# Performance work log

Hardware: AMD Instinct MI355X
Metric: run time of the kernel (lower is better)

## Reference

```python
import jax, jax.numpy as jnp
import numpy as np

N_NODES = 50000
N_EDGES = 200000
NODE_F = 64
EDGE_F = 16
HID = 32
LAT = 16


def _glorot(key, shape):
    fan_in, fan_out = shape[0], shape[1]
    lim = np.sqrt(6.0 / (fan_in + fan_out))
    return jax.random.uniform(key, shape, jnp.float32, -lim, lim)


def setup_inputs() -> dict:
    key = jax.random.key(0)
    ks = jax.random.split(key, 24)
    inp = {
        "x": jax.random.normal(ks[0], (N_NODES, NODE_F), jnp.float32),
        "edge_index": jax.random.randint(ks[1], (2, N_EDGES), 0, N_NODES, jnp.int64),
        "edge_attr": jax.random.normal(ks[2], (N_EDGES, EDGE_F), jnp.float32),
        # encoder input projection
        "lin_in_w": _glorot(ks[3], (NODE_F, HID)),
        "lin_in_b": jnp.zeros((HID,), jnp.float32),
        # 3 edge MLPs (stacked over layer axis)
        "edge_w1": jnp.stack([_glorot(ks[4 + i], (EDGE_F, HID)) for i in range(3)]),
        "edge_b1": jnp.zeros((3, HID), jnp.float32),
        "edge_w2": jnp.stack([_glorot(ks[7 + i], (HID, HID * HID)) * 0.1 for i in range(3)]),
        "edge_b2": jnp.zeros((3, HID * HID), jnp.float32),
        # 3 NNConv root weights + biases
        "root_w": jnp.stack([_glorot(ks[10 + i], (HID, HID)) for i in range(3)]),
        "root_b": jnp.zeros((3, HID), jnp.float32),
        # encoder output projection
        "lin_out_w": _glorot(ks[13], (HID, LAT)),
        "lin_out_b": jnp.zeros((LAT,), jnp.float32),
        # node decoder MLP
        "dec_w1": _glorot(ks[14], (LAT, HID)),
        "dec_b1": jnp.zeros((HID,), jnp.float32),
        "dec_w2": _glorot(ks[15], (HID, NODE_F)),
        "dec_b2": jnp.zeros((NODE_F,), jnp.float32),
    }
    return inp


def _nnconv(x, src, dst, edge_attr, w1, b1, w2, b2, root_w, root_b):
    # per-edge weight matrix from edge MLP: [E, H, H]
    h = jax.nn.relu(edge_attr @ w1 + b1)
    w_e = (h @ w2 + b2).reshape(-1, HID, HID)
    # gather source features, per-edge matmul: [E, H]
    msg = jnp.einsum("eh,eho->eo", x[src], w_e)
    # scatter-mean to destinations
    agg = jax.ops.segment_sum(msg, dst, num_segments=N_NODES)
    cnt = jax.ops.segment_sum(jnp.ones((msg.shape[0], 1), x.dtype), dst, num_segments=N_NODES)
    agg = agg / jnp.maximum(cnt, 1.0)
    # root weight + bias
    return agg + x @ root_w + root_b


def reference(x, edge_index, edge_attr, lin_in_w, lin_in_b, edge_w1, edge_b1,
              edge_w2, edge_b2, root_w, root_b, lin_out_w, lin_out_b,
              dec_w1, dec_b1, dec_w2, dec_b2):
    src, dst = edge_index[0], edge_index[1]
    h = jax.nn.relu(x @ lin_in_w + lin_in_b)
    for i in range(3):  # fixed number of conv layers (dropout is identity in eval)
        h = _nnconv(h, src, dst, edge_attr, edge_w1[i], edge_b1[i],
                    edge_w2[i], edge_b2[i], root_w[i], root_b[i])
        h = jax.nn.relu(h)
    z = h @ lin_out_w + lin_out_b
    # node decoder
    d = jax.nn.relu(z @ dec_w1 + dec_b1)
    return d @ dec_w2 + dec_b2
```

## Files before the change

kernel.cpp:

```cpp
#include <hip/hip_runtime.h>
#include <hip/hip_bf16.h>
#include <stdint.h>

#define N_NODES 50000
#define N_EDGES 200000
#define NODE_F 64
#define EDGE_F 16
#define HID 32
#define LAT 16
#define KTOT 1056
#define SCAN_BLOCKS 196

typedef __attribute__((ext_vector_type(8))) short short8;
typedef __attribute__((ext_vector_type(4))) float f32x4;
typedef __attribute__((ext_vector_type(2))) float f32x2;

static __device__ __forceinline__ unsigned short bfbits(float f) {
  union { __hip_bfloat16 h; unsigned short s; } c; c.h = __float2bfloat16(f); return c.s;
}
static __device__ __forceinline__ unsigned pkt(f32x2 v) {
  return __builtin_amdgcn_perm(__float_as_uint(v.y), __float_as_uint(v.x), 0x07060302u);
}
union AFrag { short8 v; unsigned u[4]; };

__global__ void k_prep(const float* __restrict__ ew2, const float* __restrict__ eb2,
                       const float* __restrict__ ew1,
                       unsigned short* __restrict__ w2t,
                       unsigned short* __restrict__ w1p,
                       int* __restrict__ deg) {
  int g = blockIdx.x*256 + threadIdx.x;
  int l = g / (HID*KTOT);
  int r = g % (HID*KTOT);
  int o = r / KTOT;
  int kg = r % KTOT;
  int k = kg >> 5, h = kg & 31;
  float v = (k < 32) ? ew2[(size_t)l*32768 + k*1024 + h*32 + o]
                     : eb2[(size_t)l*1024 + h*32 + o];
  w2t[g] = bfbits(v);
  if (g < N_NODES) deg[g] = 0;
  if (g < 3*2*64*8) {
    int l2 = g >> 10;
    int r2 = g & 1023;
    int nt = r2 >> 9;
    int ln = (r2 >> 3) & 63;
    int j  = r2 & 7;
    int kgr = ln >> 4;
    float w = (kgr < 2) ? ew1[(size_t)l2*512 + (kgr*8 + j)*32 + nt*16 + (ln & 15)] : 0.f;
    w1p[g] = bfbits(w);
  }
}

__global__ void k_hist(const int* __restrict__ ei, int* __restrict__ deg) {
  int t = blockIdx.x*256 + threadIdx.x;
  if (t >= N_EDGES) return;
  int d = ei[N_EDGES + t];
  d = min(max(d, 0), N_NODES-1);
  atomicAdd(&deg[d], 1);
}

__global__ __launch_bounds__(256) void k_scan1(const int* __restrict__ deg,
                                               int* __restrict__ off,
                                               int* __restrict__ bsum) {
  __shared__ int s[256];
  const int tid = threadIdx.x;
  const int t = blockIdx.x*256 + tid;
  int d = (t < N_NODES) ? deg[t] : 0;
  s[tid] = d; __syncthreads();
  int v = d;
  #pragma unroll
  for (int ofs = 1; ofs < 256; ofs <<= 1) {
    int w = (tid >= ofs) ? s[tid-ofs] : 0;
    __syncthreads();
    v += w; s[tid] = v;
    __syncthreads();
  }
  if (t < N_NODES) off[t] = v - d;
  if (tid == 255) bsum[blockIdx.x] = v;
}

__global__ __launch_bounds__(256) void k_scan23(int* __restrict__ off,
                                                const int* __restrict__ bsum,
                                                int* __restrict__ cursor) {
  __shared__ int sPref;
  const int tid = threadIdx.x;
  const int b = blockIdx.x;
  if (tid < 64) {
    int acc = 0;
    for (int i = tid; i < b; i += 64) acc += bsum[i];
    #pragma unroll
    for (int o = 32; o; o >>= 1) acc += __shfl_down(acc, o);
    if (tid == 0) sPref = acc;
  }
  __syncthreads();
  int pref = sPref;
  int t = b*256 + tid;
  if (t < N_NODES) {
    off[t] += pref;
    cursor[t] = 0;
  }
  if (t == 0) off[N_NODES] = N_EDGES;
}

__global__ void k_scatter(const int* __restrict__ ei, const int* __restrict__ off,
                          int* __restrict__ cursor, int* __restrict__ csr_pos) {
  int t = blockIdx.x*256 + threadIdx.x;
  if (t >= N_EDGES) return;
  int d = ei[N_EDGES + t];
  d = min(max(d, 0), N_NODES-1);
  int pos = atomicAdd(&cursor[d], 1);
  csr_pos[t] = off[d] + pos;
}

__global__ void k_lin_in(const float* __restrict__ x,
                         const float* __restrict__ W,
                         const float* __restrict__ b,
                         float* __restrict__ h) {
  __shared__ float Ws[NODE_F*HID];
  __shared__ float bs[HID];
  for (int i = threadIdx.x; i < NODE_F*HID; i += 256) Ws[i] = W[i];
  if (threadIdx.x < HID) bs[threadIdx.x] = b[threadIdx.x];
  __syncthreads();
  int t = blockIdx.x*256 + threadIdx.x;
  if (t >= N_NODES*HID) return;
  int n = t >> 5, o = t & 31;
  const float4* xp = (const float4*)(x + (size_t)n*NODE_F);
  float acc = bs[o];
  #pragma unroll
  for (int j = 0; j < NODE_F/4; j++) {
    float4 v = xp[j];
    acc = fmaf(v.x, Ws[(4*j+0)*HID+o], acc);
    acc = fmaf(v.y, Ws[(4*j+1)*HID+o], acc);
    acc = fmaf(v.z, Ws[(4*j+2)*HID+o], acc);
    acc = fmaf(v.w, Ws[(4*j+3)*HID+o], acc);
  }
  h[t] = fmaxf(acc, 0.f);
}

__global__ __launch_bounds__(256) void k_msg(const float* __restrict__ hin,
                                             const float* __restrict__ ea,
                                             const int* __restrict__ ei,
                                             const unsigned short* __restrict__ w1pl,
                                             const float* __restrict__ b1,
                                             const unsigned short* __restrict__ w2tl,
                                             const int* __restrict__ csr_pos,
                                             unsigned short* __restrict__ msgB) {
  __shared__ float sHE[256*33];
  __shared__ int   sSRC[256];
  __shared__ int   sPOS[256];
  const int tid = threadIdx.x;
  const int be  = blockIdx.x*256;
  const int wv   = tid >> 6;
  const int lane = tid & 63;
  const int nn   = lane & 15;
  const int quad = lane >> 4;
  const int wbase = wv*64;

  {
    int el = wbase + lane;
    int e = min(be + el, N_EDGES-1);
    sSRC[el] = min(max(ei[e], 0), N_NODES-1);
    sPOS[el] = csr_pos[e];
    sHE[el*33 + 32] = 1.0f;
  }

  {
    short8 wb0 = *(const short8*)(w1pl + lane*8);
    short8 wb1 = *(const short8*)(w1pl + 512 + lane*8);
    f32x4 z = {0.f,0.f,0.f,0.f};
    float bv0 = b1[nn], bv1 = b1[nn + 16];
    #pragma unroll
    for (int t = 0; t < 4; t++) {
      AFrag a;
      if (quad < 2) {
        int e = min(be + wbase + t*16 + nn, N_EDGES-1);
        const float4* p = (const float4*)(ea + (size_t)e*EDGE_F + quad*8);
        float4 u = p[0], v = p[1];
        a.u[0] = pkt(f32x2{u.x,u.y}); a.u[1] = pkt(f32x2{u.z,u.w});
        a.u[2] = pkt(f32x2{v.x,v.y}); a.u[3] = pkt(f32x2{v.z,v.w});
      } else {
        #pragma unroll
        for (int i = 0; i < 4; i++) a.u[i] = 0u;
      }
      f32x4 h0 = __builtin_amdgcn_mfma_f32_16x16x32_bf16(a.v, wb0, z, 0, 0, 0);
      f32x4 h1 = __builtin_amdgcn_mfma_f32_16x16x32_bf16(a.v, wb1, z, 0, 0, 0);
      #pragma unroll
      for (int r = 0; r < 4; r++) {
        int ro = (wbase + t*16 + quad*4 + r)*33;
        sHE[ro + nn]      = fmaxf(h0[r] + bv0, 0.f);
        sHE[ro + 16 + nn] = fmaxf(h1[r] + bv1, 0.f);
      }
    }
  }

  f32x2 xs[4][4];
  #pragma unroll
  for (int t = 0; t < 4; t++) {
    int si = sSRC[wbase + t*16 + nn];
    const float4* p = (const float4*)(hin + (size_t)si*HID);
    float4 a = p[quad*2], b = p[quad*2+1];
    xs[t][0] = f32x2{a.x, a.y}; xs[t][1] = f32x2{a.z, a.w};
    xs[t][2] = f32x2{b.x, b.y}; xs[t][3] = f32x2{b.z, b.w};
  }

  f32x4 c0[4], c1[4];
  #pragma unroll
  for (int t = 0; t < 4; t++) { c0[t] = f32x4{0.f,0.f,0.f,0.f}; c1[t] = c0[t]; }

  const unsigned short* bp0 = w2tl + (unsigned)nn*KTOT + quad*8;
  const unsigned short* bp1 = bp0 + 16*KTOT;
  const float* heR[4];
  #pragma unroll
  for (int t = 0; t < 4; t++) heR[t] = sHE + (wbase + t*16 + nn)*33;

  short8 sb0[3], sb1[3];
  float  sh[3][4];
  #pragma unroll
  for (int j = 0; j < 3; j++) {
    sb0[j] = *(const short8*)(bp0 + j*32);
    sb1[j] = *(const short8*)(bp1 + j*32);
    #pragma unroll
    for (int t = 0; t < 4; t++) sh[j][t] = heR[t][j];
  }

  #pragma unroll 1
  for (int base = 0; base < 30; base += 3) {
    #pragma unroll
    for (int j = 0; j < 3; j++) {
      const int kk = base + j;
      short8 cb0 = sb0[j], cb1 = sb1[j];
      #pragma unroll
      for (int t = 0; t < 4; t++) {
        float hk = sh[j][t];
        AFrag a;
        #pragma unroll
        for (int i = 0; i < 4; i++) a.u[i] = pkt(xs[t][i]*hk);
        c0[t] = __builtin_amdgcn_mfma_f32_16x16x32_bf16(a.v, cb0, c0[t], 0, 0, 0);
        c1[t] = __builtin_amdgcn_mfma_f32_16x16x32_bf16(a.v, cb1, c1[t], 0, 0, 0);
      }
      sb0[j] = *(const short8*)(bp0 + (kk+3)*32);
      sb1[j] = *(const short8*)(bp1 + (kk+3)*32);
      #pragma unroll
      for (int t = 0; t < 4; t++) sh[j][t] = heR[t][kk+3];
    }
  }
  #pragma unroll
  for (int j = 0; j < 3; j++) {
    short8 cb0 = sb0[j], cb1 = sb1[j];
    #pragma unroll
    for (int t = 0; t < 4; t++) {
      float hk = sh[j][t];
      AFrag a;
      #pragma unroll
      for (int i = 0; i < 4; i++) a.u[i] = pkt(xs[t][i]*hk);
      c0[t] = __builtin_amdgcn_mfma_f32_16x16x32_bf16(a.v, cb0, c0[t], 0, 0, 0);
      c1[t] = __builtin_amdgcn_mfma_f32_16x16x32_bf16(a.v, cb1, c1[t], 0, 0, 0);
    }
  }

  #pragma unroll
  for (int t = 0; t < 4; t++) {
    #pragma unroll
    for (int r = 0; r < 4; r++) {
      int el = wbase + t*16 + quad*4 + r;
      if (be + el < N_EDGES) {
        size_t row = (size_t)sPOS[el]*HID;
        msgB[row +      nn] = bfbits(c0[t][r]);
        msgB[row + 16 + nn] = bfbits(c1[t][r]);
      }
    }
  }
}

__global__ void k_gather(const unsigned short* __restrict__ msgB,
                         const int* __restrict__ off,
                         const float* __restrict__ hin,
                         const float* __restrict__ rw,
                         const float* __restrict__ rb,
                         float* __restrict__ hout) {
  __shared__ float rws[HID*HID];
  __shared__ float rbs[HID];
  for (int i = threadIdx.x; i < HID*HID; i += 256) rws[i] = rw[i];
  if (threadIdx.x < HID) rbs[threadIdx.x] = rb[threadIdx.x];
  __syncthreads();
  int t = blockIdx.x*256 + threadIdx.x;
  if (t >= N_NODES*8) return;
  int n = t >> 3, oc = t & 7;
  int s0 = off[n], s1 = off[n+1];
  float a0 = 0.f, a1 = 0.f, a2 = 0.f, a3 = 0.f;
  for (int j = s0; j < s1; j++) {
    uint2 u = *(const uint2*)(msgB + (size_t)j*HID + oc*4);
    a0 += __uint_as_float(u.x << 16);
    a1 += __uint_as_float(u.x & 0xffff0000u);
    a2 += __uint_as_float(u.y << 16);
    a3 += __uint_as_float(u.y & 0xffff0000u);
  }
  float inv = 1.f / fmaxf((float)(s1 - s0), 1.f);
  a0 = fmaf(a0, inv, rbs[oc*4+0]);
  a1 = fmaf(a1, inv, rbs[oc*4+1]);
  a2 = fmaf(a2, inv, rbs[oc*4+2]);
  a3 = fmaf(a3, inv, rbs[oc*4+3]);
  const float4* hp = (const float4*)(hin + (size_t)n*HID);
  #pragma unroll
  for (int jq = 0; jq < 8; jq++) {
    float4 hv = hp[jq];
    #pragma unroll
    for (int c = 0; c < 4; c++) {
      int j = jq*4 + c;
      float h = (c==0)?hv.x:(c==1)?hv.y:(c==2)?hv.z:hv.w;
      const float4* rp = (const float4*)(rws + j*HID + oc*4);
      float4 r = rp[0];
      a0 = fmaf(h, r.x, a0);
      a1 = fmaf(h, r.y, a1);
      a2 = fmaf(h, r.z, a2);
      a3 = fmaf(h, r.w, a3);
    }
  }
  float4 res = make_float4(fmaxf(a0,0.f), fmaxf(a1,0.f), fmaxf(a2,0.f), fmaxf(a3,0.f));
  ((float4*)(hout + (size_t)n*HID))[oc] = res;
}

__global__ void k_decoder(const float* __restrict__ h,
                          const float* __restrict__ lo_w, const float* __restrict__ lo_b,
                          const float* __restrict__ d1_w, const float* __restrict__ d1_b,
                          const float* __restrict__ d2_w, const float* __restrict__ d2_b,
                          float* __restrict__ out) {
  __shared__ float lows[HID*LAT], lobs[LAT], d1s[LAT*HID], d1bs[HID], d2s[HID*NODE_F], d2bs[NODE_F];
  for (int i = threadIdx.x; i < HID*LAT; i += 256) lows[i] = lo_w[i];
  for (int i = threadIdx.x; i < LAT; i += 256) lobs[i] = lo_b[i];
  for (int i = threadIdx.x; i < LAT*HID; i += 256) d1s[i] = d1_w[i];
  for (int i = threadIdx.x; i < HID; i += 256) d1bs[i] = d1_b[i];
  for (int i = threadIdx.x; i < HID*NODE_F; i += 256) d2s[i] = d2_w[i];
  for (int i = threadIdx.x; i < NODE_F; i += 256) d2bs[i] = d2_b[i];
  __syncthreads();
  int n = blockIdx.x*256 + threadIdx.x;
  if (n >= N_NODES) return;
  float hr[HID];
  const float4* hp = (const float4*)(h + (size_t)n*HID);
  #pragma unroll
  for (int i = 0; i < HID/4; i++) { float4 v = hp[i]; hr[4*i]=v.x; hr[4*i+1]=v.y; hr[4*i+2]=v.z; hr[4*i+3]=v.w; }
  float z[LAT];
  #pragma unroll
  for (int o = 0; o < LAT; o++) {
    float a = lobs[o];
    #pragma unroll
    for (int j = 0; j < HID; j++) a = fmaf(hr[j], lows[j*LAT+o], a);
    z[o] = a;
  }
  float d[HID];
  #pragma unroll
  for (int o = 0; o < HID; o++) {
    float a = d1bs[o];
    #pragma unroll
    for (int j = 0; j < LAT; j++) a = fmaf(z[j], d1s[j*HID+o], a);
    d[o] = fmaxf(a, 0.f);
  }
  float* op = out + (size_t)n*NODE_F;
  #pragma unroll 8
  for (int o = 0; o < NODE_F; o++) {
    float a = d2bs[o];
    #pragma unroll
    for (int j = 0; j < HID; j++) a = fmaf(d[j], d2s[j*NODE_F+o], a);
    op[o] = a;
  }
}

extern "C" void kernel_launch(void* const* d_in, const int* in_sizes, int n_in,
                              void* d_out, int out_size, void* d_ws, size_t ws_size,
                              hipStream_t stream) {
  const float* x   = (const float*)d_in[0];
  const int*   ei  = (const int*)d_in[1];
  const float* ea  = (const float*)d_in[2];
  const float* liw = (const float*)d_in[3];
  const float* lib = (const float*)d_in[4];
  const float* ew1 = (const float*)d_in[5];
  const float* eb1 = (const float*)d_in[6];
  const float* ew2 = (const float*)d_in[7];
  const float* eb2 = (const float*)d_in[8];
  const float* rw  = (const float*)d_in[9];
  const float* rb  = (const float*)d_in[10];
  const float* low = (const float*)d_in[11];
  const float* lob = (const float*)d_in[12];
  const float* d1w = (const float*)d_in[13];
  const float* d1b = (const float*)d_in[14];
  const float* d2w = (const float*)d_in[15];
  const float* d2b = (const float*)d_in[16];
  float* out = (float*)d_out;

  float* h0   = (float*)d_ws;
  float* h1   = h0  + (size_t)N_NODES*HID;
  unsigned short* msgB = (unsigned short*)(h1 + (size_t)N_NODES*HID);
  int*  deg   = (int*)(msgB + (size_t)N_EDGES*HID);
  int*  off   = deg + N_NODES;
  int*  cursor= off + N_NODES + 16;
  int*  cpos  = cursor + N_NODES;
  int*  bsum  = cpos + N_EDGES;
  unsigned short* w2t = (unsigned short*)(bsum + 256);
  unsigned short* w1p = w2t + 3*HID*KTOT;

  k_prep<<<(3*HID*KTOT)/256, 256, 0, stream>>>(ew2, eb2, ew1, w2t, w1p, deg);
  k_hist<<<(N_EDGES + 255)/256, 256, 0, stream>>>(ei, deg);
  k_scan1<<<SCAN_BLOCKS, 256, 0, stream>>>(deg, off, bsum);
  k_scan23<<<SCAN_BLOCKS, 256, 0, stream>>>(off, bsum, cursor);
  k_scatter<<<(N_EDGES + 255)/256, 256, 0, stream>>>(ei, off, cursor, cpos);

  k_lin_in<<<(N_NODES*HID + 255)/256, 256, 0, stream>>>(x, liw, lib, h0);

  float* hin = h0; float* hout = h1;
  for (int i = 0; i < 3; i++) {
    k_msg<<<(N_EDGES + 255)/256, 256, 0, stream>>>(hin, ea, ei,
        w1p + (size_t)i*1024, eb1 + i*HID,
        w2t + (size_t)i*HID*KTOT, cpos, msgB);
    k_gather<<<(N_NODES*8 + 255)/256, 256, 0, stream>>>(msgB, off, hin,
        rw + i*HID*HID, rb + i*HID, hout);
    float* t = hin; hin = hout; hout = t;
  }

  k_decoder<<<(N_NODES + 255)/256, 256, 0, stream>>>(hin, low, lob, d1w, d1b, d2w, d2b, out);
}
```

Before: 276.3 us.

## Reorder per-edge message contraction: MFMA over weights times x, then scale by h

The per-edge message is recomputed as a sum over k of h_k times (W2_k^T x), with W2 as the A operand and the gathered source features as a fixed B fragment. This replaces the per-k scaling and bf16 packing of x by h_k with FMAs on the MFMA outputs, using MFMA with a zero accumulator. The weight layout is rebuilt in prep to match the A-fragment format, and message stores become packed 8-byte writes. In exchange it adds VALU FMAs per MFMA output element, and the extra dependency on each MFMA result could stall the pipeline.

Measured after the change: 282.7 us. 2.3% more time.

```diff
diff --git a/kernel.cpp b/kernel.cpp
--- a/kernel.cpp
+++ b/kernel.cpp
@@ -9,6 +9,7 @@
 #define HID 32
 #define LAT 16
 #define KTOT 1056
+#define W2A_L 33792
 #define SCAN_BLOCKS 196
 
 typedef __attribute__((ext_vector_type(8))) short short8;
@@ -25,27 +26,31 @@
 
 __global__ void k_prep(const float* __restrict__ ew2, const float* __restrict__ eb2,
                        const float* __restrict__ ew1,
-                       unsigned short* __restrict__ w2t,
+                       unsigned short* __restrict__ w2a,
                        unsigned short* __restrict__ w1p,
                        int* __restrict__ deg) {
   int g = blockIdx.x*256 + threadIdx.x;
-  int l = g / (HID*KTOT);
-  int r = g % (HID*KTOT);
-  int o = r / KTOT;
-  int kg = r % KTOT;
-  int k = kg >> 5, h = kg & 31;
-  float v = (k < 32) ? ew2[(size_t)l*32768 + k*1024 + h*32 + o]
-                     : eb2[(size_t)l*1024 + h*32 + o];
-  w2t[g] = bfbits(v);
+  int l = g / W2A_L;
+  int r = g % W2A_L;
+  int k = r >> 10;
+  int r2 = r & 1023;
+  int mt = r2 >> 9;
+  int ln = (r2 >> 3) & 63;
+  int j  = r2 & 7;
+  int h  = (ln >> 4)*8 + j;
+  int m  = mt*16 + (ln & 15);
+  float v = (k < 32) ? ew2[(size_t)l*32768 + k*1024 + h*32 + m]
+                     : eb2[(size_t)l*1024 + h*32 + m];
+  w2a[g] = bfbits(v);
   if (g < N_NODES) deg[g] = 0;
   if (g < 3*2*64*8) {
     int l2 = g >> 10;
-    int r2 = g & 1023;
-    int nt = r2 >> 9;
-    int ln = (r2 >> 3) & 63;
-    int j  = r2 & 7;
-    int kgr = ln >> 4;
-    float w = (kgr < 2) ? ew1[(size_t)l2*512 + (kgr*8 + j)*32 + nt*16 + (ln & 15)] : 0.f;
+    int r3 = g & 1023;
+    int nt = r3 >> 9;
+    int ln2 = (r3 >> 3) & 63;
+    int j2  = r3 & 7;
+    int kgr = ln2 >> 4;
+    float w = (kgr < 2) ? ew1[(size_t)l2*512 + (kgr*8 + j2)*32 + nt*16 + (ln2 & 15)] : 0.f;
     w1p[g] = bfbits(w);
   }
 }
@@ -141,7 +146,7 @@
                                              const int* __restrict__ ei,
                                              const unsigned short* __restrict__ w1pl,
                                              const float* __restrict__ b1,
-                                             const unsigned short* __restrict__ w2tl,
+                                             const unsigned short* __restrict__ w2al,
                                              const int* __restrict__ csr_pos,
                                              unsigned short* __restrict__ msgB) {
   __shared__ float sHE[256*33];
@@ -192,32 +197,34 @@
     }
   }
 
-  f32x2 xs[4][4];
+  short8 bx[4];
   #pragma unroll
   for (int t = 0; t < 4; t++) {
     int si = sSRC[wbase + t*16 + nn];
-    const float4* p = (const float4*)(hin + (size_t)si*HID);
-    float4 a = p[quad*2], b = p[quad*2+1];
-    xs[t][0] = f32x2{a.x, a.y}; xs[t][1] = f32x2{a.z, a.w};
-    xs[t][2] = f32x2{b.x, b.y}; xs[t][3] = f32x2{b.z, b.w};
+    const float4* p = (const float4*)(hin + (size_t)si*HID + quad*8);
+    float4 a = p[0], b = p[1];
+    AFrag f;
+    f.u[0] = pkt(f32x2{a.x,a.y}); f.u[1] = pkt(f32x2{a.z,a.w});
+    f.u[2] = pkt(f32x2{b.x,b.y}); f.u[3] = pkt(f32x2{b.z,b.w});
+    bx[t] = f.v;
   }
 
   f32x4 c0[4], c1[4];
   #pragma unroll
   for (int t = 0; t < 4; t++) { c0[t] = f32x4{0.f,0.f,0.f,0.f}; c1[t] = c0[t]; }
-
-  const unsigned short* bp0 = w2tl + (unsigned)nn*KTOT + quad*8;
-  const unsigned short* bp1 = bp0 + 16*KTOT;
+  const f32x4 zz = {0.f,0.f,0.f,0.f};
+
+  const unsigned short* ap = w2al + (unsigned)lane*8;
   const float* heR[4];
   #pragma unroll
   for (int t = 0; t < 4; t++) heR[t] = sHE + (wbase + t*16 + nn)*33;
 
-  short8 sb0[3], sb1[3];
+  short8 sa0[3], sa1[3];
   float  sh[3][4];
   #pragma unroll
   for (int j = 0; j < 3; j++) {
-    sb0[j] = *(const short8*)(bp0 + j*32);
-    sb1[j] = *(const short8*)(bp1 + j*32);
+    sa0[j] = *(const short8*)(ap + j*1024);
+    sa1[j] = *(const short8*)(ap + j*1024 + 512);
     #pragma unroll
     for (int t = 0; t < 4; t++) sh[j][t] = heR[t][j];
   }
@@ -227,46 +234,51 @@
     #pragma unroll
     for (int j = 0; j < 3; j++) {
       const int kk = base + j;
-      short8 cb0 = sb0[j], cb1 = sb1[j];
+      short8 a0 = sa0[j], a1 = sa1[j];
       #pragma unroll
       for (int t = 0; t < 4; t++) {
+        f32x4 u0 = __builtin_amdgcn_mfma_f32_16x16x32_bf16(a0, bx[t], zz, 0, 0, 0);
+        f32x4 u1 = __builtin_amdgcn_mfma_f32_16x16x32_bf16(a1, bx[t], zz, 0, 0, 0);
         float hk = sh[j][t];
-        AFrag a;
         #pragma unroll
-        for (int i = 0; i < 4; i++) a.u[i] = pkt(xs[t][i]*hk);
-        c0[t] = __builtin_amdgcn_mfma_f32_16x16x32_bf16(a.v, cb0, c0[t], 0, 0, 0);
-        c1[t] = __builtin_amdgcn_mfma_f32_16x16x32_bf16(a.v, cb1, c1[t], 0, 0, 0);
+        for (int r = 0; r < 4; r++) {
+          c0[t][r] = fmaf(hk, u0[r], c0[t][r]);
+          c1[t][r] = fmaf(hk, u1[r], c1[t][r]);
+        }
       }
-      sb0[j] = *(const short8*)(bp0 + (kk+3)*32);
-      sb1[j] = *(const short8*)(bp1 + (kk+3)*32);
+      sa0[j] = *(const short8*)(ap + (kk+3)*1024);
+      sa1[j] = *(const short8*)(ap + (kk+3)*1024 + 512);
       #pragma unroll
       for (int t = 0; t < 4; t++) sh[j][t] = heR[t][kk+3];
     }
   }
   #pragma unroll
   for (int j = 0; j < 3; j++) {
-    short8 cb0 = sb0[j], cb1 = sb1[j];
+    short8 a0 = sa0[j], a1 = sa1[j];
     #pragma unroll
     for (int t = 0; t < 4; t++) {
+      f32x4 u0 = __builtin_amdgcn_mfma_f32_16x16x32_bf16(a0, bx[t], zz, 0, 0, 0);
+      f32x4 u1 = __builtin_amdgcn_mfma_f32_16x16x32_bf16(a1, bx[t], zz, 0, 0, 0);
       float hk = sh[j][t];
-      AFrag a;
       #pragma unroll
-      for (int i = 0; i < 4; i++) a.u[i] = pkt(xs[t][i]*hk);
-      c0[t] = __builtin_amdgcn_mfma_f32_16x16x32_bf16(a.v, cb0, c0[t], 0, 0, 0);
-      c1[t] = __builtin_amdgcn_mfma_f32_16x16x32_bf16(a.v, cb1, c1[t], 0, 0, 0);
+      for (int r = 0; r < 4; r++) {
+        c0[t][r] = fmaf(hk, u0[r], c0[t][r]);
+        c1[t][r] = fmaf(hk, u1[r], c1[t][r]);
+      }
     }
   }
 
   #pragma unroll
   for (int t = 0; t < 4; t++) {
-    #pragma unroll
-    for (int r = 0; r < 4; r++) {
-      int el = wbase + t*16 + quad*4 + r;
-      if (be + el < N_EDGES) {
-        size_t row = (size_t)sPOS[el]*HID;
-        msgB[row +      nn] = bfbits(c0[t][r]);
-        msgB[row + 16 + nn] = bfbits(c1[t][r]);
-      }
+    int el = wbase + t*16 + nn;
+    if (be + el < N_EDGES) {
+      size_t row = (size_t)sPOS[el]*HID;
+      unsigned a0 = bfbits(c0[t][0]) | ((unsigned)bfbits(c0[t][1]) << 16);
+      unsigned a1 = bfbits(c0[t][2]) | ((unsigned)bfbits(c0[t][3]) << 16);
+      unsigned b0 = bfbits(c1[t][0]) | ((unsigned)bfbits(c1[t][1]) << 16);
+      unsigned b1v = bfbits(c1[t][2]) | ((unsigned)bfbits(c1[t][3]) << 16);
+      *(uint2*)(msgB + row + quad*4)      = make_uint2(a0, a1);
+      *(uint2*)(msgB + row + 16 + quad*4) = make_uint2(b0, b1v);
     }
   }
 }
@@ -394,10 +406,10 @@
   int*  cursor= off + N_NODES + 16;
   int*  cpos  = cursor + N_NODES;
   int*  bsum  = cpos + N_EDGES;
-  unsigned short* w2t = (unsigned short*)(bsum + 256);
-  unsigned short* w1p = w2t + 3*HID*KTOT;
-
-  k_prep<<<(3*HID*KTOT)/256, 256, 0, stream>>>(ew2, eb2, ew1, w2t, w1p, deg);
+  unsigned short* w2a = (unsigned short*)(bsum + 256);
+  unsigned short* w1p = w2a + 3*W2A_L;
+
+  k_prep<<<(3*W2A_L)/256, 256, 0, stream>>>(ew2, eb2, ew1, w2a, w1p, deg);
   k_hist<<<(N_EDGES + 255)/256, 256, 0, stream>>>(ei, deg);
   k_scan1<<<SCAN_BLOCKS, 256, 0, stream>>>(deg, off, bsum);
   k_scan23<<<SCAN_BLOCKS, 256, 0, stream>>>(off, bsum, cursor);
@@ -409,7 +421,7 @@
   for (int i = 0; i < 3; i++) {
     k_msg<<<(N_EDGES + 255)/256, 256, 0, stream>>>(hin, ea, ei,
         w1p + (size_t)i*1024, eb1 + i*HID,
-        w2t + (size_t)i*HID*KTOT, cpos, msgB);
+        w2a + (size_t)i*W2A_L, cpos, msgB);
     k_gather<<<(N_NODES*8 + 255)/256, 256, 0, stream>>>(msgB, off, hin,
         rw + i*HID*HID, rb + i*HID, hout);
     float* t = hin; hin = hout; hout = t;
```
